# Optimization experiments

Measured on AMD Instinct MI355X. Metric: run time of the kernel, lower is better.

The kernel has to match this reference:

```python
import jax, jax.numpy as jnp
import numpy as np

B, T, D, H, DK, FF, V, L = 2, 1024, 768, 12, 64, 3072, 50257, 12


def setup_inputs() -> dict:
    key = jax.random.key(0)
    ks = jax.random.split(key, 9)
    s = 0.02  # matches nn.init.normal_(std=0.02)
    rn = lambda k, sh: jax.random.normal(k, sh, jnp.float32) * s
    return {
        "x": jax.random.randint(ks[0], (B, T), 0, V),
        "tok_emb": rn(ks[1], (V, D)),
        "pos_emb": rn(ks[2], (T, D)),
        "Wq": rn(ks[3], (L, D, D)), "bq": jnp.zeros((L, D), jnp.float32),
        "Wk": rn(ks[4], (L, D, D)), "bk": jnp.zeros((L, D), jnp.float32),
        "Wv": rn(ks[5], (L, D, D)), "bv": jnp.zeros((L, D), jnp.float32),
        "Wo": rn(ks[6], (L, D, D)), "bo": jnp.zeros((L, D), jnp.float32),
        "ln1_g": jnp.ones((L, D), jnp.float32), "ln1_b": jnp.zeros((L, D), jnp.float32),
        "ln2_g": jnp.ones((L, D), jnp.float32), "ln2_b": jnp.zeros((L, D), jnp.float32),
        "W1": rn(ks[7], (L, D, FF)), "b1": jnp.zeros((L, FF), jnp.float32),
        "W2": rn(ks[8], (L, FF, D)), "b2": jnp.zeros((L, D), jnp.float32),
        "lnf_g": jnp.ones((D,), jnp.float32), "lnf_b": jnp.zeros((D,), jnp.float32),
    }


def _ln(x, g, b, eps=1e-5):
    m = jnp.mean(x, axis=-1, keepdims=True)
    v = jnp.var(x, axis=-1, keepdims=True)  # biased var, like torch LayerNorm
    return (x - m) * jax.lax.rsqrt(v + eps) * g + b


def _forward(x, tok_emb, pos_emb, Wq, bq, Wk, bk, Wv, bv, Wo, bo,
             ln1_g, ln1_b, ln2_g, ln2_b, W1, b1, W2, b2, lnf_g, lnf_b):
    Bsz, Tn = x.shape
    h = tok_emb[x] + pos_emb[:Tn][None]  # [B,T,D]
    causal = jnp.tril(jnp.ones((Tn, Tn), dtype=bool))  # True = keep
    scale = 1.0 / np.sqrt(DK)

    def block(h, p):
        wq, bq_, wk, bk_, wv, bv_, wo, bo_, g1, be1, g2, be2, w1, bf1, w2, bf2 = p
        x2 = _ln(h, g1, be1)
        q = (x2 @ wq + bq_).reshape(Bsz, Tn, H, DK)
        k = (x2 @ wk + bk_).reshape(Bsz, Tn, H, DK)
        v = (x2 @ wv + bv_).reshape(Bsz, Tn, H, DK)
        scores = jnp.einsum("bqhd,bkhd->bhqk", q, k) * scale
        scores = jnp.where(causal, scores, -jnp.inf)
        attn = jax.nn.softmax(scores, axis=-1)  # dropout is identity in eval
        ctx = jnp.einsum("bhqk,bkhd->bqhd", attn, v).reshape(Bsz, Tn, D)
        h = h + ctx @ wo + bo_
        x2 = _ln(h, g2, be2)
        ff = jax.nn.gelu(x2 @ w1 + bf1, approximate=False) @ w2 + bf2  # exact GELU like F.gelu
        return h + ff, None

    params = (Wq, bq, Wk, bk, Wv, bv, Wo, bo, ln1_g, ln1_b, ln2_g, ln2_b, W1, b1, W2, b2)
    h, _ = jax.lax.scan(block, h, params)
    h = _ln(h, lnf_g, lnf_b)
    return h @ tok_emb.T  # tied lm_head, [B,T,V]


def reference(x, tok_emb, pos_emb, Wq, bq, Wk, bk, Wv, bv, Wo, bo,
              ln1_g, ln1_b, ln2_g, ln2_b, W1, b1, W2, b2, lnf_g, lnf_b):
    return _forward(x, tok_emb, pos_emb, Wq, bq, Wk, bk, Wv, bv, Wo, bo,
                    ln1_g, ln1_b, ln2_g, ln2_b, W1, b1, W2, b2, lnf_g, lnf_b)
```

## Files before the change

### kernel.cpp

```cpp
#include <hip/hip_runtime.h>
#include <cmath>

#define DI __device__ __forceinline__

typedef unsigned short u16;
typedef __bf16 bf16x8 __attribute__((ext_vector_type(8)));
typedef float f32x4 __attribute__((ext_vector_type(4)));

static constexpr int Bsz = 2, T = 1024, D = 768, H = 12, FF = 3072, V = 50257, L = 12;
static constexpr int M = Bsz * T;
static constexpr int QKVS = 3 * D;

DI u16 f2bf(float f) {
  unsigned u = __float_as_uint(f);
  u = (u + 0x7fffu + ((u >> 16) & 1u)) >> 16;
  return (u16)u;
}
DI float bf2f(u16 h) { return __uint_as_float(((unsigned)h) << 16); }

DI void gload_lds16(const void* g, void* l) {
  __builtin_amdgcn_global_load_lds((const __attribute__((address_space(1))) void*)g,
                                   (__attribute__((address_space(3))) void*)l, 16, 0, 0);
}

__launch_bounds__(256)
__global__ void transpose_cvt(const float* __restrict__ src, u16* __restrict__ dst, int R, int C) {
  __shared__ float tile[32][33];
  const int tx = threadIdx.x, ty = threadIdx.y;
  const int c0 = blockIdx.x * 32, r0 = blockIdx.y * 32;
  src += (size_t)blockIdx.z * R * C;
  dst += (size_t)blockIdx.z * R * C;
#pragma unroll
  for (int i = 0; i < 4; ++i)
    tile[ty + i * 8][tx] = src[(size_t)(r0 + ty + i * 8) * C + c0 + tx];
  __syncthreads();
#pragma unroll
  for (int i = 0; i < 4; ++i)
    dst[(size_t)(c0 + ty + i * 8) * R + r0 + tx] = f2bf(tile[tx][ty + i * 8]);
}

__launch_bounds__(256)
__global__ void transpose_qkvo(const float* __restrict__ Wq, const float* __restrict__ Wk,
                               const float* __restrict__ Wv, const float* __restrict__ Wo,
                               u16* __restrict__ wqkvT, u16* __restrict__ woT) {
  __shared__ float tile[32][33];
  const int tx = threadIdx.x, ty = threadIdx.y;
  const int c0 = blockIdx.x * 32, r0 = blockIdx.y * 32;
  const int z = blockIdx.z, mat = z / L, layer = z % L;
  const float* srcs[4] = {Wq, Wk, Wv, Wo};
  const float* src = srcs[mat] + (size_t)layer * D * D;
  u16* dst = (mat < 3) ? wqkvT + (size_t)layer * 3 * D * D + (size_t)mat * D * D
                       : woT + (size_t)layer * D * D;
#pragma unroll
  for (int i = 0; i < 4; ++i)
    tile[ty + i * 8][tx] = src[(size_t)(r0 + ty + i * 8) * D + c0 + tx];
  __syncthreads();
#pragma unroll
  for (int i = 0; i < 4; ++i)
    dst[(size_t)(c0 + ty + i * 8) * D + r0 + tx] = f2bf(tile[tx][ty + i * 8]);
}

__launch_bounds__(256)
__global__ void fuse_bias(const float* __restrict__ bq, const float* __restrict__ bk,
                          const float* __restrict__ bv, float* __restrict__ out) {
  const int l = blockIdx.y;
  const int j = blockIdx.x * 256 + threadIdx.x;
  float v;
  if (j < 768) v = bq[l * 768 + j];
  else if (j < 1536) v = bk[l * 768 + j - 768];
  else v = bv[l * 768 + j - 1536];
  out[(size_t)l * QKVS + j] = v;
}

__global__ void convert_bf16(const float* __restrict__ src, u16* __restrict__ dst, long n4) {
  long i = (long)blockIdx.x * blockDim.x + threadIdx.x;
  long stride = (long)gridDim.x * blockDim.x;
  for (; i < n4; i += stride) {
    float4 f = ((const float4*)src)[i];
    ushort4 o;
    o.x = f2bf(f.x); o.y = f2bf(f.y); o.z = f2bf(f.z); o.w = f2bf(f.w);
    ((ushort4*)dst)[i] = o;
  }
}

__launch_bounds__(256)
__global__ void embed_kernel(const int* __restrict__ x, const float* __restrict__ tok,
                             const float* __restrict__ pos, float* __restrict__ h) {
  const int row = blockIdx.x, t = threadIdx.x;
  const int tt = row % T;
  const int id = x[row];
  float* o = h + (size_t)row * D;
  const float* te = tok + (size_t)id * D;
  const float* pe = pos + (size_t)tt * D;
  o[t] = te[t] + pe[t];
  o[t + 256] = te[t + 256] + pe[t + 256];
  o[t + 512] = te[t + 512] + pe[t + 512];
}

__launch_bounds__(256)
__global__ void layernorm_kernel(const float* __restrict__ in, const float* __restrict__ gw,
                                 const float* __restrict__ bw, u16* __restrict__ out) {
  const int lane = threadIdx.x & 63, wid = threadIdx.x >> 6;
  const int row = blockIdx.x * 4 + wid;
  const float4* x4 = (const float4*)(in + (size_t)row * D);
  float4 v[3];
  float sum = 0.f, sq = 0.f;
#pragma unroll
  for (int j = 0; j < 3; ++j) {
    v[j] = x4[lane + 64 * j];
    sum += v[j].x + v[j].y + v[j].z + v[j].w;
    sq += v[j].x * v[j].x + v[j].y * v[j].y + v[j].z * v[j].z + v[j].w * v[j].w;
  }
#pragma unroll
  for (int off = 1; off < 64; off <<= 1) {
    sum += __shfl_xor(sum, off);
    sq += __shfl_xor(sq, off);
  }
  const float mean = sum * (1.0f / D);
  const float var = sq * (1.0f / D) - mean * mean;
  const float rstd = rsqrtf(var + 1e-5f);
  const float4* g4 = (const float4*)gw;
  const float4* b4 = (const float4*)bw;
  ushort4* o4 = (ushort4*)(out + (size_t)row * D);
#pragma unroll
  for (int j = 0; j < 3; ++j) {
    float4 g = g4[lane + 64 * j], b = b4[lane + 64 * j];
    ushort4 o;
    o.x = f2bf((v[j].x - mean) * rstd * g.x + b.x);
    o.y = f2bf((v[j].y - mean) * rstd * g.y + b.y);
    o.z = f2bf((v[j].z - mean) * rstd * g.z + b.z);
    o.w = f2bf((v[j].w - mean) * rstd * g.w + b.w);
    o4[lane + 64 * j] = o;
  }
}

template <int EPI, int BM, int BN, int BK>
DI void gemm_core(const u16* __restrict__ A, const u16* __restrict__ Bt,
                  const float* bias, float* outF, u16* outH, const float* resid,
                  int N, int K, int m0, int n0) {
  __shared__ u16 sA[BM * BK];
  __shared__ u16 sB[BN * BK];
  constexpr int FM = BM / 32, FN = BN / 32;
  constexpr int CPR = BK / 8;
  constexpr int KS = BK / 32;
  constexpr int AI = BM * BK / 8 / 256;
  constexpr int BI = BN * BK / 8 / 256;
  const int t = threadIdx.x;
  const int lane = t & 63, wid = t >> 6;

  f32x4 acc[FM][FN] = {};
  const int wr = (wid >> 1) * (BM / 2), wc = (wid & 1) * (BN / 2);
  const int rsel = lane & 15, ksel = lane >> 4;

  for (int k0 = 0; k0 < K; k0 += BK) {
#pragma unroll
    for (int i = 0; i < AI; ++i) {
      int c = t + i * 256;
      int row = c / CPR, ch = c % CPR;
      int g = ch ^ (row & (CPR - 1));
      gload_lds16(A + (size_t)(m0 + row) * K + k0 + g * 8, &sA[c * 8]);
    }
#pragma unroll
    for (int i = 0; i < BI; ++i) {
      int c = t + i * 256;
      int row = c / CPR, ch = c % CPR;
      int g = ch ^ (row & (CPR - 1));
      int nr = n0 + row;
      if (nr >= N) nr = N - 1;
      gload_lds16(Bt + (size_t)nr * K + k0 + g * 8, &sB[c * 8]);
    }
    __syncthreads();
#pragma unroll
    for (int ks = 0; ks < KS; ++ks) {
      bf16x8 af[FM], bfr[FN];
#pragma unroll
      for (int m = 0; m < FM; ++m) {
        int row = wr + m * 16 + rsel;
        int ch = (ksel + 4 * ks) ^ (row & (CPR - 1));
        af[m] = *(const bf16x8*)&sA[row * BK + ch * 8];
      }
#pragma unroll
      for (int n = 0; n < FN; ++n) {
        int row = wc + n * 16 + rsel;
        int ch = (ksel + 4 * ks) ^ (row & (CPR - 1));
        bfr[n] = *(const bf16x8*)&sB[row * BK + ch * 8];
      }
#pragma unroll
      for (int m = 0; m < FM; ++m)
#pragma unroll
        for (int n = 0; n < FN; ++n)
          acc[m][n] = __builtin_amdgcn_mfma_f32_16x16x32_bf16(af[m], bfr[n], acc[m][n], 0, 0, 0);
    }
    __syncthreads();
  }

  const int rq = lane >> 4;
#pragma unroll
  for (int m = 0; m < FM; ++m) {
#pragma unroll
    for (int n = 0; n < FN; ++n) {
      const int col = n0 + wc + n * 16 + rsel;
      if (col >= N) continue;
      const float bv = bias ? bias[col] : 0.0f;
#pragma unroll
      for (int i = 0; i < 4; ++i) {
        const int row = m0 + wr + m * 16 + rq * 4 + i;
        float v = acc[m][n][i] + bv;
        const size_t idx = (size_t)row * N + col;
        if (EPI == 0) {
          outH[idx] = f2bf(v);
        } else if (EPI == 1) {
          float ge = 0.5f * v * (1.0f + erff(v * 0.70710678118f));
          outH[idx] = f2bf(ge);
        } else if (EPI == 2) {
          outF[idx] = resid[idx] + v;
        } else {
          outF[idx] = v;
        }
      }
    }
  }
}

__launch_bounds__(256) __global__ void gemm_qkv(const u16* __restrict__ A, const u16* __restrict__ Bt,
                                                const float* bias, u16* out) {
  gemm_core<0, 128, 64, 64>(A, Bt, bias, nullptr, out, nullptr, QKVS, D,
                            blockIdx.x * 128, blockIdx.y * 64);
}
__launch_bounds__(256) __global__ void gemm_proj(const u16* __restrict__ A, const u16* __restrict__ Bt,
                                                 const float* bias, float* h) {
  gemm_core<2, 64, 64, 64>(A, Bt, bias, h, nullptr, h, D, D, blockIdx.x * 64, blockIdx.y * 64);
}
__launch_bounds__(256) __global__ void gemm_ff1(const u16* __restrict__ A, const u16* __restrict__ Bt,
                                                const float* bias, u16* out) {
  gemm_core<1, 128, 64, 64>(A, Bt, bias, nullptr, out, nullptr, FF, D,
                            blockIdx.x * 128, blockIdx.y * 64);
}
__launch_bounds__(256) __global__ void gemm_ff2(const u16* __restrict__ A, const u16* __restrict__ Bt,
                                                const float* bias, float* h) {
  gemm_core<2, 64, 64, 128>(A, Bt, bias, h, nullptr, h, D, FF, blockIdx.x * 64, blockIdx.y * 64);
}
__launch_bounds__(256) __global__ void gemm_lm(const u16* __restrict__ A, const u16* __restrict__ Bt,
                                               float* out) {
  const int flat = blockIdx.y * gridDim.x + blockIdx.x;
  const int nwg = gridDim.x * gridDim.y;
  const int cpx = nwg >> 3;
  const int nf = (flat & 7) * cpx + (flat >> 3);
  const int m0 = (nf & 15) * 128, n0 = (nf >> 4) * 128;
  gemm_core<3, 128, 128, 32>(A, Bt, nullptr, out, nullptr, nullptr, V, D, m0, n0);
}

__launch_bounds__(256)
__global__ void attn_mfma(const u16* __restrict__ qkv, u16* __restrict__ ctx) {
  __shared__ u16 sK[64 * 64];
  __shared__ u16 sVT[64 * 72];
  __shared__ u16 sP[4][16 * 72];
  const int t = threadIdx.x, lane = t & 63, wid = t >> 6;
  const int l15 = lane & 15, g = lane >> 4;
  const int qc = gridDim.x - 1 - blockIdx.x;
  const int q0 = qc * 64;
  const int bh = blockIdx.y;
  const int b = bh / H, hh = bh % H;
  const size_t rowbase = (size_t)b * T;
  u16* sPw = &sP[wid][0];

  const size_t qoff = (rowbase + q0 + wid * 16 + l15) * QKVS + hh * 64 + g * 8;
  bf16x8 aQ0 = *(const bf16x8*)&qkv[qoff];
  bf16x8 aQ1 = *(const bf16x8*)&qkv[qoff + 32];
#pragma unroll
  for (int j = 0; j < 8; ++j) {
    aQ0[j] = (__bf16)(0.125f * (float)aQ0[j]);
    aQ1[j] = (__bf16)(0.125f * (float)aQ1[j]);
  }

  float mr[4] = {-INFINITY, -INFINITY, -INFINITY, -INFINITY};
  float lr[4] = {0.f, 0.f, 0.f, 0.f};
  f32x4 o[4] = {};
  const int nt = qc + 1;

  for (int kt = 0; kt < nt; ++kt) {
    __syncthreads();
#pragma unroll
    for (int i = 0; i < 2; ++i) {
      int c = t + i * 256;
      int row = c >> 3, ch = c & 7;
      gload_lds16(qkv + (rowbase + kt * 64 + row) * QKVS + D + hh * 64 +
                      (size_t)((ch ^ (row & 7)) * 8),
                  &sK[c * 8]);
    }
    {
      const int a = t & 31, d0 = (t >> 5) * 8;
      const size_t vrow = (rowbase + kt * 64 + 2 * a) * QKVS + 2 * D + hh * 64 + d0;
      bf16x8 vA = *(const bf16x8*)&qkv[vrow];
      bf16x8 vB = *(const bf16x8*)&qkv[vrow + QKVS];
#pragma unroll
      for (int j = 0; j < 8; ++j) {
        ushort2 w;
        w.x = ((u16*)&vA)[j];
        w.y = ((u16*)&vB)[j];
        *(ushort2*)&sVT[(d0 + j) * 72 + 2 * a] = w;
      }
    }
    __syncthreads();

    f32x4 s[4];
    __builtin_amdgcn_s_setprio(1);
#pragma unroll
    for (int f = 0; f < 4; ++f) {
      const int krow = f * 16 + l15;
      bf16x8 bk0 = *(const bf16x8*)&sK[krow * 64 + ((g ^ (krow & 7)) * 8)];
      bf16x8 bk1 = *(const bf16x8*)&sK[krow * 64 + (((g + 4) ^ (krow & 7)) * 8)];
      f32x4 z = {};
      z = __builtin_amdgcn_mfma_f32_16x16x32_bf16(aQ0, bk0, z, 0, 0, 0);
      s[f] = __builtin_amdgcn_mfma_f32_16x16x32_bf16(aQ1, bk1, z, 0, 0, 0);
    }
    __builtin_amdgcn_s_setprio(0);

    float p[4][4], scl[4];
    const bool diag = (kt == qc);
#pragma unroll
    for (int i = 0; i < 4; ++i) {
      float v0 = s[0][i], v1 = s[1][i], v2 = s[2][i], v3 = s[3][i];
      if (diag) {
        const int qrow = q0 + wid * 16 + g * 4 + i;
        const int kb = kt * 64 + l15;
        v0 = (kb <= qrow) ? v0 : -INFINITY;
        v1 = (kb + 16 <= qrow) ? v1 : -INFINITY;
        v2 = (kb + 32 <= qrow) ? v2 : -INFINITY;
        v3 = (kb + 48 <= qrow) ? v3 : -INFINITY;
      }
      float mt = fmaxf(fmaxf(v0, v1), fmaxf(v2, v3));
#pragma unroll
      for (int off = 1; off < 16; off <<= 1) mt = fmaxf(mt, __shfl_xor(mt, off));
      const float mn = fmaxf(mr[i], mt);
      const float sc = __expf(mr[i] - mn);
      p[0][i] = __expf(v0 - mn); p[1][i] = __expf(v1 - mn);
      p[2][i] = __expf(v2 - mn); p[3][i] = __expf(v3 - mn);
      float rs = p[0][i] + p[1][i] + p[2][i] + p[3][i];
#pragma unroll
      for (int off = 1; off < 16; off <<= 1) rs += __shfl_xor(rs, off);
      lr[i] = lr[i] * sc + rs;
      mr[i] = mn;
      scl[i] = sc;
    }
#pragma unroll
    for (int n = 0; n < 4; ++n) {
      o[n][0] *= scl[0]; o[n][1] *= scl[1]; o[n][2] *= scl[2]; o[n][3] *= scl[3];
    }
#pragma unroll
    for (int f = 0; f < 4; ++f)
#pragma unroll
      for (int i = 0; i < 4; ++i)
        sPw[(g * 4 + i) * 72 + f * 16 + l15] = f2bf(p[f][i]);

    __builtin_amdgcn_s_setprio(1);
#pragma unroll
    for (int kb = 0; kb < 2; ++kb) {
      bf16x8 pa = *(const bf16x8*)&sPw[l15 * 72 + kb * 32 + g * 8];
#pragma unroll
      for (int n = 0; n < 4; ++n) {
        bf16x8 bv = *(const bf16x8*)&sVT[(n * 16 + l15) * 72 + kb * 32 + g * 8];
        o[n] = __builtin_amdgcn_mfma_f32_16x16x32_bf16(pa, bv, o[n], 0, 0, 0);
      }
    }
    __builtin_amdgcn_s_setprio(0);
  }

  float inv[4] = {1.0f / lr[0], 1.0f / lr[1], 1.0f / lr[2], 1.0f / lr[3]};
#pragma unroll
  for (int n = 0; n < 4; ++n)
#pragma unroll
    for (int i = 0; i < 4; ++i)
      ctx[(rowbase + q0 + wid * 16 + g * 4 + i) * D + hh * 64 + n * 16 + l15] =
          f2bf(o[n][i] * inv[i]);
}

extern "C" void kernel_launch(void* const* d_in, const int* in_sizes, int n_in,
                              void* d_out, int out_size, void* d_ws, size_t ws_size,
                              hipStream_t stream) {
  (void)in_sizes; (void)n_in; (void)out_size;
  const int* x = (const int*)d_in[0];
  const float* tok = (const float*)d_in[1];
  const float* pos = (const float*)d_in[2];
  const float* Wq = (const float*)d_in[3];
  const float* bq = (const float*)d_in[4];
  const float* Wk = (const float*)d_in[5];
  const float* bk = (const float*)d_in[6];
  const float* Wv = (const float*)d_in[7];
  const float* bv = (const float*)d_in[8];
  const float* Wo = (const float*)d_in[9];
  const float* bo = (const float*)d_in[10];
  const float* ln1_g = (const float*)d_in[11];
  const float* ln1_b = (const float*)d_in[12];
  const float* ln2_g = (const float*)d_in[13];
  const float* ln2_b = (const float*)d_in[14];
  const float* W1 = (const float*)d_in[15];
  const float* b1 = (const float*)d_in[16];
  const float* W2 = (const float*)d_in[17];
  const float* b2 = (const float*)d_in[18];
  const float* lnf_g = (const float*)d_in[19];
  const float* lnf_b = (const float*)d_in[20];

  char* ws = (char*)d_ws;
  size_t off = 0;
  auto alloc = [&](size_t bytes) {
    void* p = ws + off;
    off += (bytes + 255) & ~(size_t)255;
    return p;
  };
  u16* wqkvT = (u16*)alloc((size_t)L * 3 * D * D * 2);
  u16* woT   = (u16*)alloc((size_t)L * D * D * 2);
  u16* w1T   = (u16*)alloc((size_t)L * D * FF * 2);
  u16* w2T   = (u16*)alloc((size_t)L * FF * D * 2);
  u16* tokT  = (u16*)alloc((size_t)V * D * 2);
  float* bQKV = (float*)alloc((size_t)L * QKVS * 4);
  float* h   = (float*)alloc((size_t)M * D * 4);
  u16* x2    = (u16*)alloc((size_t)M * D * 2);
  u16* qkv   = (u16*)alloc((size_t)M * QKVS * 2);
  u16* ctx   = (u16*)alloc((size_t)M * D * 2);
  u16* ffb   = (u16*)alloc((size_t)M * FF * 2);
  u16* hf    = (u16*)alloc((size_t)M * D * 2);
  if (off > ws_size) return;

  const dim3 tb(32, 8);
  transpose_qkvo<<<dim3(D / 32, D / 32, 4 * L), tb, 0, stream>>>(Wq, Wk, Wv, Wo, wqkvT, woT);
  transpose_cvt<<<dim3(FF / 32, D / 32, L), tb, 0, stream>>>(W1, w1T, D, FF);
  transpose_cvt<<<dim3(D / 32, FF / 32, L), tb, 0, stream>>>(W2, w2T, FF, D);
  convert_bf16<<<2048, 256, 0, stream>>>(tok, tokT, (long)V * D / 4);
  fuse_bias<<<dim3(QKVS / 256, L), 256, 0, stream>>>(bq, bk, bv, bQKV);

  embed_kernel<<<M, 256, 0, stream>>>(x, tok, pos, h);

  for (int l = 0; l < L; ++l) {
    layernorm_kernel<<<M / 4, 256, 0, stream>>>(h, ln1_g + (size_t)l * D, ln1_b + (size_t)l * D, x2);
    gemm_qkv<<<dim3(M / 128, QKVS / 64), 256, 0, stream>>>(
        x2, wqkvT + (size_t)l * 3 * D * D, bQKV + (size_t)l * QKVS, qkv);
    attn_mfma<<<dim3(T / 64, Bsz * H), 256, 0, stream>>>(qkv, ctx);
    gemm_proj<<<dim3(M / 64, D / 64), 256, 0, stream>>>(ctx, woT + (size_t)l * D * D,
                                                        bo + (size_t)l * D, h);
    layernorm_kernel<<<M / 4, 256, 0, stream>>>(h, ln2_g + (size_t)l * D, ln2_b + (size_t)l * D, x2);
    gemm_ff1<<<dim3(M / 128, FF / 64), 256, 0, stream>>>(x2, w1T + (size_t)l * D * FF,
                                                         b1 + (size_t)l * FF, ffb);
    gemm_ff2<<<dim3(M / 64, D / 64), 256, 0, stream>>>(ffb, w2T + (size_t)l * FF * D,
                                                       b2 + (size_t)l * D, h);
  }

  layernorm_kernel<<<M / 4, 256, 0, stream>>>(h, lnf_g, lnf_b, hf);
  gemm_lm<<<dim3(16, 393), 256, 0, stream>>>(hf, tokT, (float*)d_out);
}
```

Before: 2.023 ms.

## Add triple-buffered async LDS pipeline for the LM-head GEMM

Introduces a gemm_pipe variant that keeps three LDS buffers in flight using global_load_lds, issuing loads two k-tiles ahead and waiting with explicit vmcnt counts before a barrier. Only the LM-head GEMM (the largest, K=768, BK=32) switches to it, aiming to hide global memory latency behind MFMA work. The epilogue is factored into a shared helper. This triples LDS usage for that kernel, which may lower occupancy, and relies on hand-counted vmcnt values. The single barrier per iteration also looks like it may not fully protect buffer reuse between iterations.

```diff
diff --git a/kernel.cpp b/kernel.cpp
--- a/kernel.cpp
+++ b/kernel.cpp
@@ -131,6 +131,20 @@
     o.z = f2bf((v[j].z - mean) * rstd * g.z + b.z);
     o.w = f2bf((v[j].w - mean) * rstd * g.w + b.w);
     o4[lane + 64 * j] = o;
+  }
+}
+
+template <int EPI>
+DI void epilogue_store(float v, size_t idx, float* outF, u16* outH, const float* resid) {
+  if (EPI == 0) {
+    outH[idx] = f2bf(v);
+  } else if (EPI == 1) {
+    float ge = 0.5f * v * (1.0f + erff(v * 0.70710678118f));
+    outH[idx] = f2bf(ge);
+  } else if (EPI == 2) {
+    outF[idx] = resid[idx] + v;
+  } else {
+    outF[idx] = v;
   }
 }
 
@@ -205,18 +219,106 @@
 #pragma unroll
       for (int i = 0; i < 4; ++i) {
         const int row = m0 + wr + m * 16 + rq * 4 + i;
-        float v = acc[m][n][i] + bv;
-        const size_t idx = (size_t)row * N + col;
-        if (EPI == 0) {
-          outH[idx] = f2bf(v);
-        } else if (EPI == 1) {
-          float ge = 0.5f * v * (1.0f + erff(v * 0.70710678118f));
-          outH[idx] = f2bf(ge);
-        } else if (EPI == 2) {
-          outF[idx] = resid[idx] + v;
-        } else {
-          outF[idx] = v;
-        }
+        epilogue_store<EPI>(acc[m][n][i] + bv, (size_t)row * N + col, outF, outH, resid);
+      }
+    }
+  }
+}
+
+template <int EPI, int BM, int BN, int BK>
+DI void gemm_pipe(const u16* __restrict__ A, const u16* __restrict__ Bt,
+                  const float* bias, float* outF, u16* outH, const float* resid,
+                  int N, int K, int m0, int n0) {
+  __shared__ u16 sA[3][BM * BK];
+  __shared__ u16 sB[3][BN * BK];
+  constexpr int FM = BM / 32, FN = BN / 32;
+  constexpr int CPR = BK / 8;
+  constexpr int KS = BK / 32;
+  constexpr int AI = BM * BK / 8 / 256;
+  constexpr int BI = BN * BK / 8 / 256;
+  const int t = threadIdx.x;
+  const int lane = t & 63, wid = t >> 6;
+
+  f32x4 acc[FM][FN] = {};
+  const int wr = (wid >> 1) * (BM / 2), wc = (wid & 1) * (BN / 2);
+  const int rsel = lane & 15, ksel = lane >> 4;
+  const int nk = K / BK;
+
+  auto stage = [&](int buf, int kt) {
+    const int k0 = kt * BK;
+#pragma unroll
+    for (int i = 0; i < AI; ++i) {
+      int c = t + i * 256;
+      int row = c / CPR, ch = c % CPR;
+      int g = ch ^ (row & (CPR - 1));
+      gload_lds16(A + (size_t)(m0 + row) * K + k0 + g * 8, &sA[buf][c * 8]);
+    }
+#pragma unroll
+    for (int i = 0; i < BI; ++i) {
+      int c = t + i * 256;
+      int row = c / CPR, ch = c % CPR;
+      int g = ch ^ (row & (CPR - 1));
+      int nr = n0 + row;
+      if (nr >= N) nr = N - 1;
+      gload_lds16(Bt + (size_t)nr * K + k0 + g * 8, &sB[buf][c * 8]);
+    }
+  };
+  auto compute = [&](int buf) {
+#pragma unroll
+    for (int ks = 0; ks < KS; ++ks) {
+      bf16x8 af[FM], bfr[FN];
+#pragma unroll
+      for (int m = 0; m < FM; ++m) {
+        int row = wr + m * 16 + rsel;
+        int ch = (ksel + 4 * ks) ^ (row & (CPR - 1));
+        af[m] = *(const bf16x8*)&sA[buf][row * BK + ch * 8];
+      }
+#pragma unroll
+      for (int n = 0; n < FN; ++n) {
+        int row = wc + n * 16 + rsel;
+        int ch = (ksel + 4 * ks) ^ (row & (CPR - 1));
+        bfr[n] = *(const bf16x8*)&sB[buf][row * BK + ch * 8];
+      }
+#pragma unroll
+      for (int m = 0; m < FM; ++m)
+#pragma unroll
+        for (int n = 0; n < FN; ++n)
+          acc[m][n] = __builtin_amdgcn_mfma_f32_16x16x32_bf16(af[m], bfr[n], acc[m][n], 0, 0, 0);
+    }
+  };
+
+  stage(0, 0);
+  stage(1, 1);
+  asm volatile("s_waitcnt vmcnt(%0)" ::"n"(AI + BI) : "memory");
+  __builtin_amdgcn_s_barrier();
+  int cur = 0;
+  for (int tt = 0; tt < nk - 2; ++tt) {
+    int nb = cur + 2;
+    if (nb >= 3) nb -= 3;
+    stage(nb, tt + 2);
+    compute(cur);
+    asm volatile("s_waitcnt vmcnt(%0)" ::"n"(AI + BI) : "memory");
+    __builtin_amdgcn_s_barrier();
+    if (++cur == 3) cur = 0;
+  }
+  compute(cur);
+  asm volatile("s_waitcnt vmcnt(0)" ::: "memory");
+  __builtin_amdgcn_s_barrier();
+  if (++cur == 3) cur = 0;
+  compute(cur);
+
+  const int rq = lane >> 4;
+#pragma unroll
+  for (int m = 0; m < FM; ++m) {
+#pragma unroll
+    for (int n = 0; n < FN; ++n) {
+      const int col = n0 + wc + n * 16 + rsel;
+      if (col >= N) continue;
+      const float bv = bias ? bias[col] : 0.0f;
+#pragma unroll
+      for (int i = 0; i < 4; ++i) {
+        const int row = m0 + wr + m * 16 + rq * 4 + i;
+        epilogue_store<EPI>(acc[m][n][i] + bv, (size_t)row * N + col, outF, outH, resid);
       }
     }
   }
@@ -247,7 +349,7 @@
   const int cpx = nwg >> 3;
   const int nf = (flat & 7) * cpx + (flat >> 3);
   const int m0 = (nf & 15) * 128, n0 = (nf >> 4) * 128;
-  gemm_core<3, 128, 128, 32>(A, Bt, nullptr, out, nullptr, nullptr, V, D, m0, n0);
+  gemm_pipe<3, 128, 128, 32>(A, Bt, nullptr, out, nullptr, nullptr, V, D, m0, n0);
 }
 
 __launch_bounds__(256)
```

Measured after the change: 2.072 ms. 2.4% more time.

## Widen LM-head GEMM tile to 128x256 with 512 threads; fold Q scaling into QKV epilogue

Applied to the files above, without the earlier changes.

The GEMM core is generalised over thread count and warp grid. The LM-head GEMM moves to 128x256 tiles with 8 waves in a 2x4 arrangement, which raises B-tile reuse and halves the number of workgroups. Separately, the 1/sqrt(dk) scaling of Q moves out of the attention kernel and into the QKV GEMM epilogue, so it is applied once per element. The larger tile raises LDS and register use per workgroup and lengthens the ragged final N tile.

```diff
diff --git a/kernel.cpp b/kernel.cpp
--- a/kernel.cpp
+++ b/kernel.cpp
@@ -134,35 +134,50 @@
   }
 }
 
-template <int EPI, int BM, int BN, int BK>
+template <int EPI>
+DI void epilogue_store(float v, size_t idx, float* outF, u16* outH, const float* resid) {
+  if (EPI == 0) {
+    outH[idx] = f2bf(v);
+  } else if (EPI == 1) {
+    float ge = 0.5f * v * (1.0f + erff(v * 0.70710678118f));
+    outH[idx] = f2bf(ge);
+  } else if (EPI == 2) {
+    outF[idx] = resid[idx] + v;
+  } else {
+    outF[idx] = v;
+  }
+}
+
+template <int EPI, int BM, int BN, int BK, int NTH, int WM, int WN>
 DI void gemm_core(const u16* __restrict__ A, const u16* __restrict__ Bt,
                   const float* bias, float* outF, u16* outH, const float* resid,
                   int N, int K, int m0, int n0) {
   __shared__ u16 sA[BM * BK];
   __shared__ u16 sB[BN * BK];
-  constexpr int FM = BM / 32, FN = BN / 32;
+  constexpr int WTM = BM / WM, WTN = BN / WN;
+  constexpr int FM = WTM / 16, FN = WTN / 16;
   constexpr int CPR = BK / 8;
   constexpr int KS = BK / 32;
-  constexpr int AI = BM * BK / 8 / 256;
-  constexpr int BI = BN * BK / 8 / 256;
+  constexpr int AI = BM * BK / 8 / NTH;
+  constexpr int BI = BN * BK / 8 / NTH;
   const int t = threadIdx.x;
   const int lane = t & 63, wid = t >> 6;
 
   f32x4 acc[FM][FN] = {};
-  const int wr = (wid >> 1) * (BM / 2), wc = (wid & 1) * (BN / 2);
+  const int wr = (wid / WN) * WTM, wc = (wid % WN) * WTN;
   const int rsel = lane & 15, ksel = lane >> 4;
 
   for (int k0 = 0; k0 < K; k0 += BK) {
 #pragma unroll
     for (int i = 0; i < AI; ++i) {
-      int c = t + i * 256;
+      int c = t + i * NTH;
       int row = c / CPR, ch = c % CPR;
       int g = ch ^ (row & (CPR - 1));
       gload_lds16(A + (size_t)(m0 + row) * K + k0 + g * 8, &sA[c * 8]);
     }
 #pragma unroll
     for (int i = 0; i < BI; ++i) {
-      int c = t + i * 256;
+      int c = t + i * NTH;
       int row = c / CPR, ch = c % CPR;
       int g = ch ^ (row & (CPR - 1));
       int nr = n0 + row;
@@ -206,17 +221,8 @@
       for (int i = 0; i < 4; ++i) {
         const int row = m0 + wr + m * 16 + rq * 4 + i;
         float v = acc[m][n][i] + bv;
-        const size_t idx = (size_t)row * N + col;
-        if (EPI == 0) {
-          outH[idx] = f2bf(v);
-        } else if (EPI == 1) {
-          float ge = 0.5f * v * (1.0f + erff(v * 0.70710678118f));
-          outH[idx] = f2bf(ge);
-        } else if (EPI == 2) {
-          outF[idx] = resid[idx] + v;
-        } else {
-          outF[idx] = v;
-        }
+        if (EPI == 4 && col < D) v *= 0.125f;
+        epilogue_store<EPI == 4 ? 0 : EPI>(v, (size_t)row * N + col, outF, outH, resid);
       }
     }
   }
@@ -224,30 +230,32 @@
 
 __launch_bounds__(256) __global__ void gemm_qkv(const u16* __restrict__ A, const u16* __restrict__ Bt,
                                                 const float* bias, u16* out) {
-  gemm_core<0, 128, 64, 64>(A, Bt, bias, nullptr, out, nullptr, QKVS, D,
-                            blockIdx.x * 128, blockIdx.y * 64);
+  gemm_core<4, 128, 64, 64, 256, 2, 2>(A, Bt, bias, nullptr, out, nullptr, QKVS, D,
+                                       blockIdx.x * 128, blockIdx.y * 64);
 }
 __launch_bounds__(256) __global__ void gemm_proj(const u16* __restrict__ A, const u16* __restrict__ Bt,
                                                  const float* bias, float* h) {
-  gemm_core<2, 64, 64, 64>(A, Bt, bias, h, nullptr, h, D, D, blockIdx.x * 64, blockIdx.y * 64);
+  gemm_core<2, 64, 64, 64, 256, 2, 2>(A, Bt, bias, h, nullptr, h, D, D,
+                                      blockIdx.x * 64, blockIdx.y * 64);
 }
 __launch_bounds__(256) __global__ void gemm_ff1(const u16* __restrict__ A, const u16* __restrict__ Bt,
                                                 const float* bias, u16* out) {
-  gemm_core<1, 128, 64, 64>(A, Bt, bias, nullptr, out, nullptr, FF, D,
-                            blockIdx.x * 128, blockIdx.y * 64);
+  gemm_core<1, 128, 64, 64, 256, 2, 2>(A, Bt, bias, nullptr, out, nullptr, FF, D,
+                                       blockIdx.x * 128, blockIdx.y * 64);
 }
 __launch_bounds__(256) __global__ void gemm_ff2(const u16* __restrict__ A, const u16* __restrict__ Bt,
                                                 const float* bias, float* h) {
-  gemm_core<2, 64, 64, 128>(A, Bt, bias, h, nullptr, h, D, FF, blockIdx.x * 64, blockIdx.y * 64);
-}
-__launch_bounds__(256) __global__ void gemm_lm(const u16* __restrict__ A, const u16* __restrict__ Bt,
+  gemm_core<2, 64, 64, 128, 256, 2, 2>(A, Bt, bias, h, nullptr, h, D, FF,
+                                       blockIdx.x * 64, blockIdx.y * 64);
+}
+__launch_bounds__(512) __global__ void gemm_lm(const u16* __restrict__ A, const u16* __restrict__ Bt,
                                                float* out) {
   const int flat = blockIdx.y * gridDim.x + blockIdx.x;
   const int nwg = gridDim.x * gridDim.y;
   const int cpx = nwg >> 3;
   const int nf = (flat & 7) * cpx + (flat >> 3);
-  const int m0 = (nf & 15) * 128, n0 = (nf >> 4) * 128;
-  gemm_core<3, 128, 128, 32>(A, Bt, nullptr, out, nullptr, nullptr, V, D, m0, n0);
+  const int m0 = (nf & 15) * 128, n0 = (nf >> 4) * 256;
+  gemm_core<3, 128, 256, 32, 512, 2, 4>(A, Bt, nullptr, out, nullptr, nullptr, V, D, m0, n0);
 }
 
 __launch_bounds__(256)
@@ -267,11 +275,6 @@
   const size_t qoff = (rowbase + q0 + wid * 16 + l15) * QKVS + hh * 64 + g * 8;
   bf16x8 aQ0 = *(const bf16x8*)&qkv[qoff];
   bf16x8 aQ1 = *(const bf16x8*)&qkv[qoff + 32];
-#pragma unroll
-  for (int j = 0; j < 8; ++j) {
-    aQ0[j] = (__bf16)(0.125f * (float)aQ0[j]);
-    aQ1[j] = (__bf16)(0.125f * (float)aQ1[j]);
-  }
 
   float mr[4] = {-INFINITY, -INFINITY, -INFINITY, -INFINITY};
   float lr[4] = {0.f, 0.f, 0.f, 0.f};
@@ -446,5 +449,5 @@
   }
 
   layernorm_kernel<<<M / 4, 256, 0, stream>>>(h, lnf_g, lnf_b, hf);
-  gemm_lm<<<dim3(16, 393), 256, 0, stream>>>(hf, tokT, (float*)d_out);
-}
+  gemm_lm<<<dim3(16, (V + 255) / 256), 512, 0, stream>>>(hf, tokT, (float*)d_out);
+}
```

Result: no change. 2.032 ms (+0.4%).
